# Kernel optimization log

Measured on AMD Instinct MI355X. Metric: run time of the kernel, lower is better.

Reference implementation:

```python
import jax, jax.numpy as jnp
import numpy as np

N_KEEP = 256      # number of retained DCT coefficients per box
MASK_LEN = 128    # reconstructed square mask side (gt_mask_len)
TOPK = 50         # boxes kept per image


def _zigzag_order(n):
    # order[i] = flat index (r*n+c) where the i-th zigzag element lives (JPEG zigzag)
    order = []
    for s in range(2 * n - 1):
        if s % 2 == 0:
            rng = range(min(s, n - 1), max(0, s - n + 1) - 1, -1)
        else:
            rng = range(max(0, s - n + 1), min(s, n - 1) + 1)
        for r in rng:
            order.append(r * n + (s - r))
    return np.asarray(order, dtype=np.int64)


def _dct_matrix(n):
    # orthonormal DCT-II matrix D; cv2.idct(Y) == D.T @ Y @ D
    k = np.arange(n)[:, None].astype(np.float64)
    m = np.arange(n)[None, :].astype(np.float64)
    D = np.cos(np.pi * (2.0 * m + 1.0) * k / (2.0 * n)) * np.sqrt(2.0 / n)
    D[0] *= np.sqrt(0.5)
    return D.astype(np.float32)

_INV_ZZ = np.argsort(_zigzag_order(MASK_LEN))  # flat[j] = padded_vec[_INV_ZZ[j]]
_DCT = _dct_matrix(MASK_LEN)


def setup_inputs() -> dict:
    key = jax.random.key(0)
    ks = jax.random.split(key, 6)
    B, Q, C, A = 32, 300, 91, 10
    return {
        "out_logits": jax.random.normal(ks[0], (B, Q, C), jnp.float32),
        "out_bbox": jax.random.uniform(ks[1], (B, Q, 4), jnp.float32),
        "out_vector": jax.random.normal(ks[2], (B, Q, N_KEEP), jnp.float32),
        "out_interms": jax.random.normal(ks[3], (B, Q, C), jnp.float32),
        "out_actions": jax.random.normal(ks[4], (B, 1, A), jnp.float32),
        "target_sizes": jax.random.randint(ks[5], (B, 2), 480, 1333, jnp.int32),
    }


def _box_cxcywh_to_xyxy(b):
    cx, cy, w, h = jnp.split(b, 4, axis=-1)
    return jnp.concatenate([cx - 0.5 * w, cy - 0.5 * h, cx + 0.5 * w, cy + 0.5 * h], axis=-1)


def reference(out_logits, out_bbox, out_vector, out_interms, out_actions, target_sizes):
    B, Q, C = out_logits.shape
    prob = jax.nn.sigmoid(out_logits)
    topk_values, topk_indexes = jax.lax.top_k(prob.reshape(B, -1), TOPK)
    scores = topk_values
    topk_boxes = topk_indexes // C          # [B, TOPK] query ids
    labels = topk_indexes % C               # [B, TOPK]

    boxes = _box_cxcywh_to_xyxy(out_bbox)
    boxes = jnp.take_along_axis(boxes, topk_boxes[:, :, None], axis=1)  # [B, TOPK, 4]

    prob_interms = jax.nn.sigmoid(out_interms)
    si = jnp.take_along_axis(prob_interms, topk_boxes[:, :, None], axis=1)  # [B, TOPK, C_int]
    labels_interms = jnp.argmax(si, axis=2)
    scores_interms = jnp.max(si, axis=2)

    prob_actions = jax.nn.softmax(out_actions[:, 0, :], axis=1)
    labels_action = jnp.argmax(prob_actions, axis=1)

    vectors = jnp.take_along_axis(out_vector, topk_boxes[:, :, None], axis=1)  # [B, TOPK, N_KEEP]

    ts = target_sizes.astype(boxes.dtype)
    img_h, img_w = ts[:, 0], ts[:, 1]
    scale_fct = jnp.stack([img_w, img_h, img_w, img_h], axis=1)
    boxes = boxes * scale_fct[:, None, :]

    # --- batched inverse zigzag + 2D IDCT + midpoint threshold ---
    pad = MASK_LEN * MASK_LEN - N_KEEP
    padded = jnp.pad(vectors, ((0, 0), (0, 0), (0, pad)))           # [B,TOPK,L*L]
    flat = padded[..., jnp.asarray(_INV_ZZ)]                         # inverse zigzag (gather)
    blocks = flat.reshape(B, TOPK, MASK_LEN, MASK_LEN)
    D = jnp.asarray(_DCT)
    re_mask = jnp.einsum('kn,bqkl,lm->bqnm', D, blocks, D)           # cv2.idct per box
    mx = jnp.max(re_mask, axis=(-2, -1), keepdims=True)
    mn = jnp.min(re_mask, axis=(-2, -1), keepdims=True)
    masks = (re_mask > 0.5 * (mx + mn)).astype(jnp.float32)          # [B,TOPK,L,L]

    return (scores, labels, boxes, masks, scores_interms, labels_interms, labels_action)
```

## Files before the change

### kernel.cpp

```cpp
#include <hip/hip_runtime.h>
#include <math.h>

#define BB 32
#define QQ 300
#define CC 91
#define TOPK 50
#define NKEEP 256
#define ML 128
#define QC (QQ * CC)
#define QC4 (QC / 4)
#define NPT4 7
#define EQCAP 256
#define NWAVE 16

#define OFF_SCORES ((size_t)0)
#define OFF_LABELS ((size_t)1600)
#define OFF_BOXES  ((size_t)3200)
#define OFF_MASKS  ((size_t)9600)
#define OFF_SI     ((size_t)26224000)
#define OFF_LI     ((size_t)26225600)
#define OFF_LA     ((size_t)26227200)

__device__ __forceinline__ uint32_t fkey(float f) {
    uint32_t u = __float_as_uint(f);
    return (u >> 31) ? ~u : (u | 0x80000000u);
}

__global__ __launch_bounds__(1024) void topk_kernel(const float* __restrict__ logits,
                                                    const float* __restrict__ bbox,
                                                    const float* __restrict__ actions,
                                                    const int* __restrict__ tsz,
                                                    float* __restrict__ out,
                                                    int* __restrict__ wsQ,
                                                    float* __restrict__ wsD,
                                                    int* __restrict__ wsZZ) {
    int b = blockIdx.x;
    int t = threadIdx.x;

    if (b == 0) {
        for (int idx = t; idx < 23 * 128; idx += 1024) {
            int k = idx >> 7, m = idx & 127;
            double v = cos((M_PI * (2.0 * (double)m + 1.0) * (double)k) / 256.0) * 0.125;
            if (k == 0) v *= sqrt(0.5);
            wsD[idx] = (float)v;
        }
        if (t < NKEEP) {
            int j = t;
            int s = 0;
            while ((s + 1) * (s + 2) / 2 <= j) ++s;
            int o = j - s * (s + 1) / 2;
            int r = (s & 1) ? o : (s - o);
            int c = s - r;
            wsZZ[j] = (r << 5) | c;
        }
    }

    __shared__ uint32_t hist[NWAVE * 256];
    __shared__ uint32_t scn[256];
    __shared__ uint32_t sPrefix;
    __shared__ int      sKth;
    __shared__ uint32_t cKey[TOPK];
    __shared__ int      cIdx[TOPK];
    __shared__ int      cntGt, cntEq;
    __shared__ int      eqBuf[EQCAP];
    __shared__ int      sMin;

    const float4* base4 = (const float4*)(logits + (size_t)b * QC);
    uint32_t key[NPT4][4];
#pragma unroll
    for (int i = 0; i < NPT4; ++i) {
        int p4 = t + 1024 * i;
        if (p4 < QC4) {
            float4 v = base4[p4];
            key[i][0] = fkey(v.x); key[i][1] = fkey(v.y);
            key[i][2] = fkey(v.z); key[i][3] = fkey(v.w);
        } else {
            key[i][0] = key[i][1] = key[i][2] = key[i][3] = 0u;
        }
    }

    if (t == 0) { cntGt = 0; cntEq = 0; }

    int lane = t & 63, w = t >> 6;
    uint32_t* myh = &hist[w * 256];

    uint32_t prefix = 0;
    int kth = TOPK;
    for (int pass = 0; pass < 4; ++pass) {
        int shift = 24 - 8 * pass;
        for (int i = t; i < NWAVE * 256; i += 1024) hist[i] = 0;
        __syncthreads();
        uint32_t pmask = (pass == 0) ? 0u : (0xFFFFFFFFu << (shift + 8));
#pragma unroll
        for (int i = 0; i < NPT4; ++i) {
#pragma unroll
            for (int c = 0; c < 4; ++c) {
                uint32_t k = key[i][c];
                if ((k & pmask) == prefix) atomicAdd(&myh[(k >> shift) & 255u], 1u);
            }
        }
        __syncthreads();
        if (t < 256) {
            uint32_t s = 0;
#pragma unroll
            for (int ww = 0; ww < NWAVE; ++ww) s += hist[ww * 256 + t];
            scn[t] = s;
        }
        __syncthreads();
        if (t < 64) {
            uint4 h4 = *(const uint4*)&scn[lane * 4];
            uint32_t s3 = h4.w;
            uint32_t s2 = h4.z + s3;
            uint32_t s1 = h4.y + s2;
            uint32_t s0 = h4.x + s1;
            uint32_t inc = s0;
#pragma unroll
            for (int off = 1; off < 64; off <<= 1) {
                uint32_t v = __shfl_down(inc, off);
                if (lane + off < 64) inc += v;
            }
            uint32_t higher = inc - s0;
            uint32_t sarr[4] = {s0, s1, s2, s3};
            uint32_t harr[4] = {h4.x, h4.y, h4.z, h4.w};
#pragma unroll
            for (int c = 0; c < 4; ++c) {
                int cge = (int)(sarr[c] + higher);
                int cgt = cge - (int)harr[c];
                if (cge >= kth && cgt < kth) {
                    sPrefix = prefix | ((uint32_t)(lane * 4 + c) << shift);
                    sKth = kth - cgt;
                }
            }
        }
        __syncthreads();
        prefix = sPrefix;
        kth = sKth;
    }

    uint32_t T = prefix;
    int need = kth;
    int cgt = TOPK - need;

#pragma unroll
    for (int i = 0; i < NPT4; ++i) {
#pragma unroll
        for (int c = 0; c < 4; ++c) {
            uint32_t k = key[i][c];
            if (k > T) {
                int pos = atomicAdd(&cntGt, 1);
                cKey[pos] = k; cIdx[pos] = 4 * (t + 1024 * i) + c;
            } else if (k == T) {
                int pos = atomicAdd(&cntEq, 1);
                if (pos < EQCAP) eqBuf[pos] = 4 * (t + 1024 * i) + c;
            }
        }
    }
    __syncthreads();

    if (cntEq <= EQCAP) {
        for (int j = t; j < cntEq; j += 1024) {
            int my = eqBuf[j];
            int rank = 0;
            for (int m = 0; m < cntEq; ++m) rank += (eqBuf[m] < my);
            if (rank < need) { cKey[cgt + rank] = T; cIdx[cgt + rank] = my; }
        }
        __syncthreads();
    } else {
        for (int r = 0; r < need; ++r) {
            if (t == 0) sMin = 0x7fffffff;
            __syncthreads();
            int loc = 0x7fffffff;
#pragma unroll
            for (int i = 0; i < NPT4; ++i)
#pragma unroll
                for (int c = 0; c < 4; ++c)
                    if (key[i][c] == T) loc = min(loc, 4 * (t + 1024 * i) + c);
            atomicMin(&sMin, loc);
            __syncthreads();
            int m = sMin;
#pragma unroll
            for (int i = 0; i < NPT4; ++i)
#pragma unroll
                for (int c = 0; c < 4; ++c)
                    if (4 * (t + 1024 * i) + c == m) key[i][c] = 0;
            if (t == 0) { cKey[cgt + r] = T; cIdx[cgt + r] = m; }
            __syncthreads();
        }
    }

    if (t < TOPK) {
        uint32_t myk = cKey[t]; int myi = cIdx[t];
        int rank = 0;
        for (int m = 0; m < TOPK; ++m) {
            uint32_t ok = cKey[m]; int oi = cIdx[m];
            rank += (ok > myk) || (ok == myk && oi < myi);
        }
        uint32_t u = (myk >> 31) ? (myk & 0x7fffffffu) : ~myk;
        float val = __uint_as_float(u);
        int q = myi / CC;
        int label = myi - q * CC;
        out[OFF_SCORES + b * TOPK + rank] = 1.0f / (1.0f + expf(-val));
        out[OFF_LABELS + b * TOPK + rank] = (float)label;
        wsQ[b * TOPK + rank] = q;
        const float* bbp = bbox + ((size_t)(b * QQ + q)) * 4;
        float cx = bbp[0], cy = bbp[1], bw = bbp[2], bh = bbp[3];
        float ih = (float)tsz[b * 2 + 0];
        float iw = (float)tsz[b * 2 + 1];
        float* bo = out + OFF_BOXES + ((size_t)(b * TOPK + rank)) * 4;
        bo[0] = (cx - 0.5f * bw) * iw;
        bo[1] = (cy - 0.5f * bh) * ih;
        bo[2] = (cx + 0.5f * bw) * iw;
        bo[3] = (cy + 0.5f * bh) * ih;
    }
    if (t == 0) {
        const float* ap = actions + (size_t)b * 10;
        float bv = ap[0]; int bi = 0;
        for (int i = 1; i < 10; ++i) { if (ap[i] > bv) { bv = ap[i]; bi = i; } }
        out[OFF_LA + b] = (float)bi;
    }
}

__global__ __launch_bounds__(256) void mask_kernel(const float* __restrict__ vec,
                                                   const float* __restrict__ interms,
                                                   const int* __restrict__ wsQ,
                                                   const float* __restrict__ wsD,
                                                   const int* __restrict__ wsZZ,
                                                   float* __restrict__ out) {
    int j = blockIdx.x;
    int b = blockIdx.y;
    int t = threadIdx.x;

    __shared__ float sD[23 * 128];
    __shared__ float sT[23 * 128];
    __shared__ float sB[23 * 24];
    __shared__ float redv[4];
    __shared__ int   redi[4];
    __shared__ float redmn[4], redmx[4];

    int q = wsQ[b * TOPK + j];

    for (int i = t; i < 23 * 128; i += 256) sD[i] = wsD[i];
    for (int i = t; i < 23 * 24; i += 256) sB[i] = 0.0f;
    __syncthreads();

    {
        int kl = wsZZ[t];
        float x = vec[((size_t)(b * QQ + q)) * NKEEP + t];
        sB[(kl >> 5) * 24 + (kl & 31)] = x;
    }

    int lane = t & 63, w = t >> 6;
    {
        float x = (t < CC) ? interms[((size_t)(b * QQ + q)) * CC + t] : -INFINITY;
        int xi = (t < CC) ? t : 0x7fffffff;
#pragma unroll
        for (int off = 32; off >= 1; off >>= 1) {
            float ov = __shfl_down(x, off);
            int   oi = __shfl_down(xi, off);
            bool better = (ov > x) || (ov == x && oi < xi);
            x = better ? ov : x;
            xi = better ? oi : xi;
        }
        if (lane == 0) { redv[w] = x; redi[w] = xi; }
    }
    __syncthreads();

    if (t == 0) {
        float gv = redv[0]; int gi = redi[0];
        for (int k = 1; k < 4; ++k) {
            bool better = (redv[k] > gv) || (redv[k] == gv && redi[k] < gi);
            gv = better ? redv[k] : gv;
            gi = better ? redi[k] : gi;
        }
        out[OFF_SI + (size_t)b * TOPK + j] = 1.0f / (1.0f + expf(-gv));
        out[OFF_LI + (size_t)b * TOPK + j] = (float)gi;
    }

    {
        int n = t & 127, h = t >> 7;
        float Dn[23];
#pragma unroll
        for (int k = 0; k < 23; ++k) Dn[k] = sD[k * 128 + n];
        for (int l = h; l < 23; l += 2) {
            float acc = 0.0f;
#pragma unroll
            for (int k = 0; k < 23; ++k) acc += Dn[k] * sB[k * 24 + l];
            sT[l * 128 + n] = acc;
        }
    }
    __syncthreads();

    int tr = t >> 4, tc = t & 15;
    float acc[8][8];
#pragma unroll
    for (int a = 0; a < 8; ++a)
#pragma unroll
        for (int c = 0; c < 8; ++c) acc[a][c] = 0.0f;

#pragma unroll
    for (int l = 0; l < 23; ++l) {
        const float4 Ta = *(const float4*)&sT[l * 128 + tr * 8];
        const float4 Tb = *(const float4*)&sT[l * 128 + tr * 8 + 4];
        const float4 Da = *(const float4*)&sD[l * 128 + tc * 8];
        const float4 Db = *(const float4*)&sD[l * 128 + tc * 8 + 4];
        float Tv[8] = {Ta.x, Ta.y, Ta.z, Ta.w, Tb.x, Tb.y, Tb.z, Tb.w};
        float Dv[8] = {Da.x, Da.y, Da.z, Da.w, Db.x, Db.y, Db.z, Db.w};
#pragma unroll
        for (int a = 0; a < 8; ++a)
#pragma unroll
            for (int c = 0; c < 8; ++c) acc[a][c] += Tv[a] * Dv[c];
    }

    float mn = acc[0][0], mx = acc[0][0];
#pragma unroll
    for (int a = 0; a < 8; ++a)
#pragma unroll
        for (int c = 0; c < 8; ++c) {
            mn = fminf(mn, acc[a][c]);
            mx = fmaxf(mx, acc[a][c]);
        }
#pragma unroll
    for (int off = 32; off >= 1; off >>= 1) {
        mn = fminf(mn, __shfl_down(mn, off));
        mx = fmaxf(mx, __shfl_down(mx, off));
    }
    if (lane == 0) { redmn[w] = mn; redmx[w] = mx; }
    __syncthreads();
    float gmn = fminf(fminf(redmn[0], redmn[1]), fminf(redmn[2], redmn[3]));
    float gmx = fmaxf(fmaxf(redmx[0], redmx[1]), fmaxf(redmx[2], redmx[3]));
    float thr = 0.5f * (gmx + gmn);

    size_t bse = OFF_MASKS + ((size_t)(b * TOPK + j)) * 16384 + (size_t)tc * 8;
#pragma unroll
    for (int a = 0; a < 8; ++a) {
        int n = tr * 8 + a;
        float4 w0 = make_float4(acc[a][0] > thr ? 1.0f : 0.0f,
                                acc[a][1] > thr ? 1.0f : 0.0f,
                                acc[a][2] > thr ? 1.0f : 0.0f,
                                acc[a][3] > thr ? 1.0f : 0.0f);
        float4 w1 = make_float4(acc[a][4] > thr ? 1.0f : 0.0f,
                                acc[a][5] > thr ? 1.0f : 0.0f,
                                acc[a][6] > thr ? 1.0f : 0.0f,
                                acc[a][7] > thr ? 1.0f : 0.0f);
        *(float4*)&out[bse + (size_t)n * 128]     = w0;
        *(float4*)&out[bse + (size_t)n * 128 + 4] = w1;
    }
}

extern "C" void kernel_launch(void* const* d_in, const int* in_sizes, int n_in,
                              void* d_out, int out_size, void* d_ws, size_t ws_size,
                              hipStream_t stream) {
    const float* logits  = (const float*)d_in[0];
    const float* bbox    = (const float*)d_in[1];
    const float* vec     = (const float*)d_in[2];
    const float* interms = (const float*)d_in[3];
    const float* actions = (const float*)d_in[4];
    const int*   tsz     = (const int*)d_in[5];
    float* out = (float*)d_out;

    float* wsD  = (float*)d_ws;
    int*   wsZZ = (int*)(wsD + 2944);
    int*   wsQ  = wsZZ + 256;

    hipLaunchKernelGGL(topk_kernel, dim3(BB), dim3(1024), 0, stream,
                       logits, bbox, actions, tsz, out, wsQ, wsD, wsZZ);
    hipLaunchKernelGGL(mask_kernel, dim3(TOPK, BB), dim3(256), 0, stream,
                       vec, interms, wsQ, wsD, wsZZ, out);
}
```

Before: 172.4 us.

## Exit radix select early with candidate sort; widen mask kernel to 512 threads

The top-k radix select now stops once the bucket holding the threshold has at most 2048 candidates. It gathers those candidates into shared memory and ranks them directly instead of always running all four histogram passes. The mask kernel now uses 512 threads per block, each computing a 4x8 output tile instead of 8x8, which lowers register pressure and raises parallelism per box. The candidate ranking is quadratic in the candidate count, and larger shared-memory arrays may reduce occupancy of the top-k kernel.

After: 233.3 us. 1.35x slower.

```diff
diff --git a/kernel.cpp b/kernel.cpp
--- a/kernel.cpp
+++ b/kernel.cpp
@@ -10,8 +10,8 @@
 #define QC (QQ * CC)
 #define QC4 (QC / 4)
 #define NPT4 7
-#define EQCAP 256
 #define NWAVE 16
+#define CAP 2048
 
 #define OFF_SCORES ((size_t)0)
 #define OFF_LABELS ((size_t)1600)
@@ -57,12 +57,13 @@
 
     __shared__ uint32_t hist[NWAVE * 256];
     __shared__ uint32_t scn[256];
-    __shared__ uint32_t sPrefix;
-    __shared__ int      sKth;
+    __shared__ uint32_t sP;
+    __shared__ int      sNeed, sCnt;
     __shared__ uint32_t cKey[TOPK];
     __shared__ int      cIdx[TOPK];
-    __shared__ int      cntGt, cntEq;
-    __shared__ int      eqBuf[EQCAP];
+    __shared__ int      cntGt, cntC;
+    __shared__ uint32_t candK[CAP];
+    __shared__ int      candI[CAP];
     __shared__ int      sMin;
 
     const float4* base4 = (const float4*)(logits + (size_t)b * QC);
@@ -79,24 +80,24 @@
         }
     }
 
-    if (t == 0) { cntGt = 0; cntEq = 0; }
+    if (t == 0) { cntGt = 0; cntC = 0; }
 
     int lane = t & 63, w = t >> 6;
     uint32_t* myh = &hist[w * 256];
 
-    uint32_t prefix = 0;
-    int kth = TOPK;
+    uint32_t P = 0, topmask = 0;
+    int need = TOPK;
+    int nCand = QC;
     for (int pass = 0; pass < 4; ++pass) {
         int shift = 24 - 8 * pass;
         for (int i = t; i < NWAVE * 256; i += 1024) hist[i] = 0;
         __syncthreads();
-        uint32_t pmask = (pass == 0) ? 0u : (0xFFFFFFFFu << (shift + 8));
 #pragma unroll
         for (int i = 0; i < NPT4; ++i) {
 #pragma unroll
             for (int c = 0; c < 4; ++c) {
                 uint32_t k = key[i][c];
-                if ((k & pmask) == prefix) atomicAdd(&myh[(k >> shift) & 255u], 1u);
+                if ((k & topmask) == P) atomicAdd(&myh[(k >> shift) & 255u], 1u);
             }
         }
         __syncthreads();
@@ -126,19 +127,19 @@
             for (int c = 0; c < 4; ++c) {
                 int cge = (int)(sarr[c] + higher);
                 int cgt = cge - (int)harr[c];
-                if (cge >= kth && cgt < kth) {
-                    sPrefix = prefix | ((uint32_t)(lane * 4 + c) << shift);
-                    sKth = kth - cgt;
+                if (cge >= need && cgt < need) {
+                    sP = P | ((uint32_t)(lane * 4 + c) << shift);
+                    sNeed = need - cgt;
+                    sCnt = (int)harr[c];
                 }
             }
         }
         __syncthreads();
-        prefix = sPrefix;
-        kth = sKth;
-    }
-
-    uint32_t T = prefix;
-    int need = kth;
+        P = sP; need = sNeed; nCand = sCnt;
+        topmask = 0xFFFFFFFFu << shift;
+        if (nCand <= CAP) break;
+    }
+
     int cgt = TOPK - need;
 
 #pragma unroll
@@ -146,23 +147,28 @@
 #pragma unroll
         for (int c = 0; c < 4; ++c) {
             uint32_t k = key[i][c];
-            if (k > T) {
+            uint32_t km = k & topmask;
+            if (km > P) {
                 int pos = atomicAdd(&cntGt, 1);
                 cKey[pos] = k; cIdx[pos] = 4 * (t + 1024 * i) + c;
-            } else if (k == T) {
-                int pos = atomicAdd(&cntEq, 1);
-                if (pos < EQCAP) eqBuf[pos] = 4 * (t + 1024 * i) + c;
-            }
-        }
-    }
-    __syncthreads();
-
-    if (cntEq <= EQCAP) {
-        for (int j = t; j < cntEq; j += 1024) {
-            int my = eqBuf[j];
+            } else if (km == P) {
+                int pos = atomicAdd(&cntC, 1);
+                if (pos < CAP) { candK[pos] = k; candI[pos] = 4 * (t + 1024 * i) + c; }
+            }
+        }
+    }
+    __syncthreads();
+
+    int nc = cntC;
+    if (nc <= CAP) {
+        for (int jj = t; jj < nc; jj += 1024) {
+            uint32_t mk = candK[jj]; int mi = candI[jj];
             int rank = 0;
-            for (int m = 0; m < cntEq; ++m) rank += (eqBuf[m] < my);
-            if (rank < need) { cKey[cgt + rank] = T; cIdx[cgt + rank] = my; }
+            for (int m = 0; m < nc; ++m) {
+                uint32_t ok = candK[m]; int oi = candI[m];
+                rank += (ok > mk) || (ok == mk && oi < mi);
+            }
+            if (rank < need) { cKey[cgt + rank] = mk; cIdx[cgt + rank] = mi; }
         }
         __syncthreads();
     } else {
@@ -174,7 +180,7 @@
             for (int i = 0; i < NPT4; ++i)
 #pragma unroll
                 for (int c = 0; c < 4; ++c)
-                    if (key[i][c] == T) loc = min(loc, 4 * (t + 1024 * i) + c);
+                    if (key[i][c] == P) loc = min(loc, 4 * (t + 1024 * i) + c);
             atomicMin(&sMin, loc);
             __syncthreads();
             int m = sMin;
@@ -183,7 +189,7 @@
 #pragma unroll
                 for (int c = 0; c < 4; ++c)
                     if (4 * (t + 1024 * i) + c == m) key[i][c] = 0;
-            if (t == 0) { cKey[cgt + r] = T; cIdx[cgt + r] = m; }
+            if (t == 0) { cKey[cgt + r] = P; cIdx[cgt + r] = m; }
             __syncthreads();
         }
     }
@@ -220,12 +226,12 @@
     }
 }
 
-__global__ __launch_bounds__(256) void mask_kernel(const float* __restrict__ vec,
-                                                   const float* __restrict__ interms,
-                                                   const int* __restrict__ wsQ,
-                                                   const float* __restrict__ wsD,
-                                                   const int* __restrict__ wsZZ,
-                                                   float* __restrict__ out) {
+__global__ __launch_bounds__(512, 8) void mask_kernel(const float* __restrict__ vec,
+                                                      const float* __restrict__ interms,
+                                                      const int* __restrict__ wsQ,
+                                                      const float* __restrict__ wsD,
+                                                      const int* __restrict__ wsZZ,
+                                                      float* __restrict__ out) {
     int j = blockIdx.x;
     int b = blockIdx.y;
     int t = threadIdx.x;
@@ -233,17 +239,17 @@
     __shared__ float sD[23 * 128];
     __shared__ float sT[23 * 128];
     __shared__ float sB[23 * 24];
-    __shared__ float redv[4];
-    __shared__ int   redi[4];
-    __shared__ float redmn[4], redmx[4];
+    __shared__ float redv[8];
+    __shared__ int   redi[8];
+    __shared__ float redmn[8], redmx[8];
 
     int q = wsQ[b * TOPK + j];
 
-    for (int i = t; i < 23 * 128; i += 256) sD[i] = wsD[i];
-    for (int i = t; i < 23 * 24; i += 256) sB[i] = 0.0f;
-    __syncthreads();
-
-    {
+    for (int i = t; i < 23 * 128; i += 512) sD[i] = wsD[i];
+    for (int i = t; i < 23 * 24; i += 512) sB[i] = 0.0f;
+    __syncthreads();
+
+    if (t < NKEEP) {
         int kl = wsZZ[t];
         float x = vec[((size_t)(b * QQ + q)) * NKEEP + t];
         sB[(kl >> 5) * 24 + (kl & 31)] = x;
@@ -267,7 +273,7 @@
 
     if (t == 0) {
         float gv = redv[0]; int gi = redi[0];
-        for (int k = 1; k < 4; ++k) {
+        for (int k = 1; k < 8; ++k) {
             bool better = (redv[k] > gv) || (redv[k] == gv && redi[k] < gi);
             gv = better ? redv[k] : gv;
             gi = better ? redi[k] : gi;
@@ -281,39 +287,38 @@
         float Dn[23];
 #pragma unroll
         for (int k = 0; k < 23; ++k) Dn[k] = sD[k * 128 + n];
-        for (int l = h; l < 23; l += 2) {
-            float acc = 0.0f;
-#pragma unroll
-            for (int k = 0; k < 23; ++k) acc += Dn[k] * sB[k * 24 + l];
-            sT[l * 128 + n] = acc;
+        for (int l = h; l < 23; l += 4) {
+            float acc1 = 0.0f;
+#pragma unroll
+            for (int k = 0; k < 23; ++k) acc1 += Dn[k] * sB[k * 24 + l];
+            sT[l * 128 + n] = acc1;
         }
     }
     __syncthreads();
 
     int tr = t >> 4, tc = t & 15;
-    float acc[8][8];
-#pragma unroll
-    for (int a = 0; a < 8; ++a)
+    float acc[4][8];
+#pragma unroll
+    for (int a = 0; a < 4; ++a)
 #pragma unroll
         for (int c = 0; c < 8; ++c) acc[a][c] = 0.0f;
 
 #pragma unroll
     for (int l = 0; l < 23; ++l) {
-        const float4 Ta = *(const float4*)&sT[l * 128 + tr * 8];
-        const float4 Tb = *(const float4*)&sT[l * 128 + tr * 8 + 4];
+        const float4 Tv4 = *(const float4*)&sT[l * 128 + tr * 4];
         const float4 Da = *(const float4*)&sD[l * 128 + tc * 8];
         const float4 Db = *(const float4*)&sD[l * 128 + tc * 8 + 4];
-        float Tv[8] = {Ta.x, Ta.y, Ta.z, Ta.w, Tb.x, Tb.y, Tb.z, Tb.w};
+        float Tv[4] = {Tv4.x, Tv4.y, Tv4.z, Tv4.w};
         float Dv[8] = {Da.x, Da.y, Da.z, Da.w, Db.x, Db.y, Db.z, Db.w};
 #pragma unroll
-        for (int a = 0; a < 8; ++a)
+        for (int a = 0; a < 4; ++a)
 #pragma unroll
             for (int c = 0; c < 8; ++c) acc[a][c] += Tv[a] * Dv[c];
     }
 
     float mn = acc[0][0], mx = acc[0][0];
 #pragma unroll
-    for (int a = 0; a < 8; ++a)
+    for (int a = 0; a < 4; ++a)
 #pragma unroll
         for (int c = 0; c < 8; ++c) {
             mn = fminf(mn, acc[a][c]);
@@ -326,14 +331,18 @@
     }
     if (lane == 0) { redmn[w] = mn; redmx[w] = mx; }
     __syncthreads();
-    float gmn = fminf(fminf(redmn[0], redmn[1]), fminf(redmn[2], redmn[3]));
-    float gmx = fmaxf(fmaxf(redmx[0], redmx[1]), fmaxf(redmx[2], redmx[3]));
+    float gmn = redmn[0], gmx = redmx[0];
+#pragma unroll
+    for (int k = 1; k < 8; ++k) {
+        gmn = fminf(gmn, redmn[k]);
+        gmx = fmaxf(gmx, redmx[k]);
+    }
     float thr = 0.5f * (gmx + gmn);
 
     size_t bse = OFF_MASKS + ((size_t)(b * TOPK + j)) * 16384 + (size_t)tc * 8;
 #pragma unroll
-    for (int a = 0; a < 8; ++a) {
-        int n = tr * 8 + a;
+    for (int a = 0; a < 4; ++a) {
+        int n = tr * 4 + a;
         float4 w0 = make_float4(acc[a][0] > thr ? 1.0f : 0.0f,
                                 acc[a][1] > thr ? 1.0f : 0.0f,
                                 acc[a][2] > thr ? 1.0f : 0.0f,
@@ -364,6 +373,6 @@
 
     hipLaunchKernelGGL(topk_kernel, dim3(BB), dim3(1024), 0, stream,
                        logits, bbox, actions, tsz, out, wsQ, wsD, wsZZ);
-    hipLaunchKernelGGL(mask_kernel, dim3(TOPK, BB), dim3(256), 0, stream,
+    hipLaunchKernelGGL(mask_kernel, dim3(TOPK, BB), dim3(512), 0, stream,
                        vec, interms, wsQ, wsD, wsZZ, out);
 }
```

## Split top-k into parallel histogram kernel and candidate-compacting select kernel

Applied to the files above, without the earlier changes.

Moves the first radix pass (top-byte histogram) into a separate kernel spread over 8 slices per image, so it no longer runs on a single 1024-thread block per batch. The select kernel then compacts the candidates in the boundary bucket into shared memory and refines only those on later passes, instead of rerunning full histograms over all keys. The aim is to cut the serial radix-select time of the 32-block top-k stage. In exchange it adds a kernel launch, a workspace round trip and a large shared candidate buffer, and keeps a fallback path for overflow.

Result: faster. 163.3 us (-5.3%).

```diff
diff --git a/kernel.cpp b/kernel.cpp
--- a/kernel.cpp
+++ b/kernel.cpp
@@ -10,8 +10,10 @@
 #define QC (QQ * CC)
 #define QC4 (QC / 4)
 #define NPT4 7
-#define EQCAP 256
 #define NWAVE 16
+#define NSLICE 8
+#define SL4 854
+#define CAP 2048
 
 #define OFF_SCORES ((size_t)0)
 #define OFF_LABELS ((size_t)1600)
@@ -26,44 +28,106 @@
     return (u >> 31) ? ~u : (u | 0x80000000u);
 }
 
-__global__ __launch_bounds__(1024) void topk_kernel(const float* __restrict__ logits,
+__device__ __forceinline__ void pick_boundary(const uint32_t* bins, int kth, int lane,
+                                              uint32_t* sBin, int* sNeed, int* sCnt) {
+    uint4 h4 = *(const uint4*)&bins[lane * 4];
+    uint32_t s3 = h4.w;
+    uint32_t s2 = h4.z + s3;
+    uint32_t s1 = h4.y + s2;
+    uint32_t s0 = h4.x + s1;
+    uint32_t inc = s0;
+#pragma unroll
+    for (int off = 1; off < 64; off <<= 1) {
+        uint32_t v = __shfl_down(inc, off);
+        if (lane + off < 64) inc += v;
+    }
+    uint32_t higher = inc - s0;
+    uint32_t sarr[4] = {s0, s1, s2, s3};
+    uint32_t harr[4] = {h4.x, h4.y, h4.z, h4.w};
+#pragma unroll
+    for (int c = 0; c < 4; ++c) {
+        int cge = (int)(sarr[c] + higher);
+        int cgt = cge - (int)harr[c];
+        if (cge >= kth && cgt < kth) {
+            *sBin = (uint32_t)(lane * 4 + c);
+            *sNeed = kth - cgt;
+            *sCnt = (int)harr[c];
+        }
+    }
+}
+
+__global__ __launch_bounds__(256) void topk_hist(const float* __restrict__ logits,
+                                                 float* __restrict__ wsD,
+                                                 int* __restrict__ wsZZ,
+                                                 uint32_t* __restrict__ wsH) {
+    int s = blockIdx.x;
+    int b = blockIdx.y;
+    int t = threadIdx.x;
+
+    if (b == 0) {
+        int lo = s * 368, hi = lo + 368;
+        if (hi > 23 * 128) hi = 23 * 128;
+        for (int idx = lo + t; idx < hi; idx += 256) {
+            int k = idx >> 7, m = idx & 127;
+            double v = cos((M_PI * (2.0 * (double)m + 1.0) * (double)k) / 256.0) * 0.125;
+            if (k == 0) v *= sqrt(0.5);
+            wsD[idx] = (float)v;
+        }
+        if (s == 0) {
+            int j = t;
+            int ss = 0;
+            while ((ss + 1) * (ss + 2) / 2 <= j) ++ss;
+            int o = j - ss * (ss + 1) / 2;
+            int r = (ss & 1) ? o : (ss - o);
+            int c = ss - r;
+            wsZZ[j] = (r << 5) | c;
+        }
+    }
+
+    __shared__ uint32_t hw[4 * 256];
+    for (int i = t; i < 4 * 256; i += 256) hw[i] = 0;
+    __syncthreads();
+
+    uint32_t* myh = &hw[(t >> 6) * 256];
+    const float4* base4 = (const float4*)(logits + (size_t)b * QC);
+    int lo4 = s * SL4;
+    int hi4 = lo4 + SL4; if (hi4 > QC4) hi4 = QC4;
+    for (int p4 = lo4 + t; p4 < hi4; p4 += 256) {
+        float4 v = base4[p4];
+        atomicAdd(&myh[fkey(v.x) >> 24], 1u);
+        atomicAdd(&myh[fkey(v.y) >> 24], 1u);
+        atomicAdd(&myh[fkey(v.z) >> 24], 1u);
+        atomicAdd(&myh[fkey(v.w) >> 24], 1u);
+    }
+    __syncthreads();
+
+    if (t < 256) {
+        uint32_t sum = hw[t] + hw[256 + t] + hw[512 + t] + hw[768 + t];
+        wsH[((size_t)(b * NSLICE + s)) * 256 + t] = sum;
+    }
+}
+
+__global__ __launch_bounds__(1024) void topk_select(const float* __restrict__ logits,
                                                     const float* __restrict__ bbox,
                                                     const float* __restrict__ actions,
                                                     const int* __restrict__ tsz,
                                                     float* __restrict__ out,
                                                     int* __restrict__ wsQ,
-                                                    float* __restrict__ wsD,
-                                                    int* __restrict__ wsZZ) {
+                                                    const uint32_t* __restrict__ wsH) {
     int b = blockIdx.x;
     int t = threadIdx.x;
-
-    if (b == 0) {
-        for (int idx = t; idx < 23 * 128; idx += 1024) {
-            int k = idx >> 7, m = idx & 127;
-            double v = cos((M_PI * (2.0 * (double)m + 1.0) * (double)k) / 256.0) * 0.125;
-            if (k == 0) v *= sqrt(0.5);
-            wsD[idx] = (float)v;
-        }
-        if (t < NKEEP) {
-            int j = t;
-            int s = 0;
-            while ((s + 1) * (s + 2) / 2 <= j) ++s;
-            int o = j - s * (s + 1) / 2;
-            int r = (s & 1) ? o : (s - o);
-            int c = s - r;
-            wsZZ[j] = (r << 5) | c;
-        }
-    }
-
-    __shared__ uint32_t hist[NWAVE * 256];
-    __shared__ uint32_t scn[256];
-    __shared__ uint32_t sPrefix;
-    __shared__ int      sKth;
+    int lane = t & 63, w = t >> 6;
+
+    __shared__ uint32_t histw[NWAVE * 256];
+    __shared__ __attribute__((aligned(16))) uint32_t h2[256];
+    __shared__ __attribute__((aligned(16))) uint32_t scn[256];
+    __shared__ uint32_t sP;
+    __shared__ int      sNeed, sCnt;
     __shared__ uint32_t cKey[TOPK];
     __shared__ int      cIdx[TOPK];
-    __shared__ int      cntGt, cntEq;
-    __shared__ int      eqBuf[EQCAP];
-    __shared__ int      sMin;
+    __shared__ int      cntTop, cntN, cntE, sMin;
+    __shared__ uint32_t candK[2][CAP];
+    __shared__ int      candI[2][CAP];
 
     const float4* base4 = (const float4*)(logits + (size_t)b * QC);
     uint32_t key[NPT4][4];
@@ -79,112 +143,168 @@
         }
     }
 
-    if (t == 0) { cntGt = 0; cntEq = 0; }
-
-    int lane = t & 63, w = t >> 6;
-    uint32_t* myh = &hist[w * 256];
-
-    uint32_t prefix = 0;
-    int kth = TOPK;
-    for (int pass = 0; pass < 4; ++pass) {
-        int shift = 24 - 8 * pass;
-        for (int i = t; i < NWAVE * 256; i += 1024) hist[i] = 0;
+    if (t < 256) {
+        uint32_t ssum = 0;
+#pragma unroll
+        for (int s = 0; s < NSLICE; ++s) ssum += wsH[((size_t)(b * NSLICE + s)) * 256 + t];
+        scn[t] = ssum;
+    }
+    if (t == 0) { cntTop = 0; cntN = 0; cntE = 0; }
+    __syncthreads();
+    if (t < 64) pick_boundary(scn, TOPK, lane, &sP, &sNeed, &sCnt);
+    __syncthreads();
+    uint32_t P0 = sP << 24;
+    int need = sNeed;
+    int nC0 = sCnt;
+
+    if (nC0 <= CAP) {
+#pragma unroll
+        for (int i = 0; i < NPT4; ++i) {
+            int p4 = t + 1024 * i;
+#pragma unroll
+            for (int c = 0; c < 4; ++c) {
+                if (p4 >= QC4) continue;
+                uint32_t k = key[i][c];
+                uint32_t hb = k & 0xFF000000u;
+                if (hb > P0) {
+                    int pos = atomicAdd(&cntTop, 1);
+                    cKey[pos] = k; cIdx[pos] = 4 * p4 + c;
+                } else if (hb == P0) {
+                    int pos = atomicAdd(&cntN, 1);
+                    candK[0][pos] = k; candI[0][pos] = 4 * p4 + c;
+                }
+            }
+        }
         __syncthreads();
-        uint32_t pmask = (pass == 0) ? 0u : (0xFFFFFFFFu << (shift + 8));
-#pragma unroll
-        for (int i = 0; i < NPT4; ++i) {
-#pragma unroll
-            for (int c = 0; c < 4; ++c) {
-                uint32_t k = key[i][c];
-                if ((k & pmask) == prefix) atomicAdd(&myh[(k >> shift) & 255u], 1u);
-            }
-        }
-        __syncthreads();
-        if (t < 256) {
-            uint32_t s = 0;
-#pragma unroll
-            for (int ww = 0; ww < NWAVE; ++ww) s += hist[ww * 256 + t];
-            scn[t] = s;
-        }
-        __syncthreads();
-        if (t < 64) {
-            uint4 h4 = *(const uint4*)&scn[lane * 4];
-            uint32_t s3 = h4.w;
-            uint32_t s2 = h4.z + s3;
-            uint32_t s1 = h4.y + s2;
-            uint32_t s0 = h4.x + s1;
-            uint32_t inc = s0;
-#pragma unroll
-            for (int off = 1; off < 64; off <<= 1) {
-                uint32_t v = __shfl_down(inc, off);
-                if (lane + off < 64) inc += v;
-            }
-            uint32_t higher = inc - s0;
-            uint32_t sarr[4] = {s0, s1, s2, s3};
-            uint32_t harr[4] = {h4.x, h4.y, h4.z, h4.w};
-#pragma unroll
-            for (int c = 0; c < 4; ++c) {
-                int cge = (int)(sarr[c] + higher);
-                int cgt = cge - (int)harr[c];
-                if (cge >= kth && cgt < kth) {
-                    sPrefix = prefix | ((uint32_t)(lane * 4 + c) << shift);
-                    sKth = kth - cgt;
-                }
-            }
-        }
-        __syncthreads();
-        prefix = sPrefix;
-        kth = sKth;
-    }
-
-    uint32_t T = prefix;
-    int need = kth;
-    int cgt = TOPK - need;
-
-#pragma unroll
-    for (int i = 0; i < NPT4; ++i) {
-#pragma unroll
-        for (int c = 0; c < 4; ++c) {
-            uint32_t k = key[i][c];
-            if (k > T) {
-                int pos = atomicAdd(&cntGt, 1);
-                cKey[pos] = k; cIdx[pos] = 4 * (t + 1024 * i) + c;
-            } else if (k == T) {
-                int pos = atomicAdd(&cntEq, 1);
-                if (pos < EQCAP) eqBuf[pos] = 4 * (t + 1024 * i) + c;
-            }
-        }
-    }
-    __syncthreads();
-
-    if (cntEq <= EQCAP) {
-        for (int j = t; j < cntEq; j += 1024) {
-            int my = eqBuf[j];
-            int rank = 0;
-            for (int m = 0; m < cntEq; ++m) rank += (eqBuf[m] < my);
-            if (rank < need) { cKey[cgt + rank] = T; cIdx[cgt + rank] = my; }
+        int nc = cntN;
+        int cur = 0;
+
+        for (int level = 1; level <= 3; ++level) {
+            if (nc <= need) break;
+            int shift = 24 - 8 * level;
+            if (t < 256) h2[t] = 0;
+            if (t == 0) cntN = 0;
+            __syncthreads();
+            for (int j2 = t; j2 < nc; j2 += 1024)
+                atomicAdd(&h2[(candK[cur][j2] >> shift) & 255u], 1u);
+            __syncthreads();
+            if (t < 64) pick_boundary(h2, need, lane, &sP, &sNeed, &sCnt);
+            __syncthreads();
+            uint32_t sub = sP;
+            int needN = sNeed;
+            for (int j2 = t; j2 < nc; j2 += 1024) {
+                uint32_t k2 = candK[cur][j2]; int i2 = candI[cur][j2];
+                uint32_t sb = (k2 >> shift) & 255u;
+                if (sb > sub) {
+                    int pos = atomicAdd(&cntTop, 1);
+                    cKey[pos] = k2; cIdx[pos] = i2;
+                } else if (sb == sub) {
+                    int pos = atomicAdd(&cntN, 1);
+                    candK[cur ^ 1][pos] = k2; candI[cur ^ 1][pos] = i2;
+                }
+            }
+            __syncthreads();
+            nc = cntN; need = needN; cur ^= 1;
+        }
+
+        int base = cntTop;
+        if (nc <= need) {
+            for (int j2 = t; j2 < nc; j2 += 1024) {
+                cKey[base + j2] = candK[cur][j2];
+                cIdx[base + j2] = candI[cur][j2];
+            }
+        } else {
+            for (int j2 = t; j2 < nc; j2 += 1024) {
+                int my = candI[cur][j2];
+                int rank = 0;
+                for (int m = 0; m < nc; ++m) rank += (candI[cur][m] < my);
+                if (rank < need) { cKey[base + rank] = candK[cur][j2]; cIdx[base + rank] = my; }
+            }
         }
         __syncthreads();
     } else {
-        for (int r = 0; r < need; ++r) {
-            if (t == 0) sMin = 0x7fffffff;
-            __syncthreads();
-            int loc = 0x7fffffff;
-#pragma unroll
-            for (int i = 0; i < NPT4; ++i)
-#pragma unroll
-                for (int c = 0; c < 4; ++c)
-                    if (key[i][c] == T) loc = min(loc, 4 * (t + 1024 * i) + c);
-            atomicMin(&sMin, loc);
-            __syncthreads();
-            int m = sMin;
-#pragma unroll
-            for (int i = 0; i < NPT4; ++i)
-#pragma unroll
-                for (int c = 0; c < 4; ++c)
-                    if (4 * (t + 1024 * i) + c == m) key[i][c] = 0;
-            if (t == 0) { cKey[cgt + r] = T; cIdx[cgt + r] = m; }
-            __syncthreads();
+        uint32_t Pfull = P0;
+        int kth = need;
+        uint32_t* myh = &histw[w * 256];
+        for (int pass = 1; pass < 4; ++pass) {
+            int shift = 24 - 8 * pass;
+            for (int i2 = t; i2 < NWAVE * 256; i2 += 1024) histw[i2] = 0;
+            __syncthreads();
+            uint32_t pmask = 0xFFFFFFFFu << (shift + 8);
+#pragma unroll
+            for (int i2 = 0; i2 < NPT4; ++i2)
+#pragma unroll
+                for (int c = 0; c < 4; ++c) {
+                    uint32_t k2 = key[i2][c];
+                    if ((k2 & pmask) == Pfull) atomicAdd(&myh[(k2 >> shift) & 255u], 1u);
+                }
+            __syncthreads();
+            if (t < 256) {
+                uint32_t ssum = 0;
+#pragma unroll
+                for (int ww = 0; ww < NWAVE; ++ww) ssum += histw[ww * 256 + t];
+                scn[t] = ssum;
+            }
+            __syncthreads();
+            if (t < 64) pick_boundary(scn, kth, lane, &sP, &sNeed, &sCnt);
+            __syncthreads();
+            Pfull |= (sP << shift);
+            kth = sNeed;
+        }
+        if (t == 0) { cntTop = 0; cntE = 0; }
+        __syncthreads();
+#pragma unroll
+        for (int i2 = 0; i2 < NPT4; ++i2) {
+            int p4 = t + 1024 * i2;
+#pragma unroll
+            for (int c = 0; c < 4; ++c) {
+                if (p4 >= QC4) continue;
+                uint32_t k2 = key[i2][c];
+                if (k2 > Pfull) {
+                    int pos = atomicAdd(&cntTop, 1);
+                    cKey[pos] = k2; cIdx[pos] = 4 * p4 + c;
+                } else if (k2 == Pfull) {
+                    int pos = atomicAdd(&cntE, 1);
+                    if (pos < CAP) candI[0][pos] = 4 * p4 + c;
+                }
+            }
+        }
+        __syncthreads();
+        int cgt2 = cntTop;
+        int ne = cntE;
+        if (ne <= CAP) {
+            for (int j2 = t; j2 < ne; j2 += 1024) {
+                int my = candI[0][j2];
+                int rank = 0;
+                for (int m = 0; m < ne; ++m) rank += (candI[0][m] < my);
+                if (rank < kth) { cKey[cgt2 + rank] = Pfull; cIdx[cgt2 + rank] = my; }
+            }
+            __syncthreads();
+        } else {
+            for (int r = 0; r < kth; ++r) {
+                if (t == 0) sMin = 0x7fffffff;
+                __syncthreads();
+                int loc = 0x7fffffff;
+#pragma unroll
+                for (int i2 = 0; i2 < NPT4; ++i2) {
+                    int p4 = t + 1024 * i2;
+#pragma unroll
+                    for (int c = 0; c < 4; ++c)
+                        if (p4 < QC4 && key[i2][c] == Pfull) loc = min(loc, 4 * p4 + c);
+                }
+                atomicMin(&sMin, loc);
+                __syncthreads();
+                int m = sMin;
+#pragma unroll
+                for (int i2 = 0; i2 < NPT4; ++i2) {
+                    int p4 = t + 1024 * i2;
+#pragma unroll
+                    for (int c = 0; c < 4; ++c)
+                        if (4 * p4 + c == m) key[i2][c] = 0;
+                }
+                if (t == 0) { cKey[cgt2 + r] = Pfull; cIdx[cgt2 + r] = m; }
+                __syncthreads();
+            }
         }
     }
 
@@ -358,12 +478,15 @@
     const int*   tsz     = (const int*)d_in[5];
     float* out = (float*)d_out;
 
-    float* wsD  = (float*)d_ws;
-    int*   wsZZ = (int*)(wsD + 2944);
-    int*   wsQ  = wsZZ + 256;
-
-    hipLaunchKernelGGL(topk_kernel, dim3(BB), dim3(1024), 0, stream,
-                       logits, bbox, actions, tsz, out, wsQ, wsD, wsZZ);
+    float*    wsD  = (float*)d_ws;
+    int*      wsZZ = (int*)(wsD + 2944);
+    int*      wsQ  = wsZZ + 256;
+    uint32_t* wsH  = (uint32_t*)(wsQ + 1600);
+
+    hipLaunchKernelGGL(topk_hist, dim3(NSLICE, BB), dim3(256), 0, stream,
+                       logits, wsD, wsZZ, wsH);
+    hipLaunchKernelGGL(topk_select, dim3(BB), dim3(1024), 0, stream,
+                       logits, bbox, actions, tsz, out, wsQ, wsH);
     hipLaunchKernelGGL(mask_kernel, dim3(TOPK, BB), dim3(256), 0, stream,
                        vec, interms, wsQ, wsD, wsZZ, out);
 }
```
